# Performance work log

Measured on AMD Instinct MI355X. Metric: run time of the kernel, lower is better.

Reference implementation:

```python
import jax, jax.numpy as jnp
import numpy as np

K = 2
ALPHA = 800.0
TAU = 0.001
MAX_ITER = 50
EPS = 1e-7


def setup_inputs() -> dict:
    key = jax.random.key(0)
    x = jax.random.normal(key, (32, 512, 128), dtype=jnp.float32)
    return {"x": x}


def _vmd(x):
    B, L, D = x.shape
    # fftshift'd frequency grid, broadcast over batch/features: [1, L, 1]
    f_shift = jnp.fft.fftshift(jnp.fft.fftfreq(L).astype(x.dtype))[None, :, None]
    pos_mask = f_shift >= 0
    f_pos = jnp.where(pos_mask, f_shift, 0.0)
    x_hat = jnp.fft.fftshift(jnp.fft.fft(x, axis=1), axes=1)  # [B, L, D] complex

    def body(carry, _):
        u, omega, lam = carry  # u:[B,K,L,D], omega:[B,K,D], lam:[B,L,D]
        # --- mode updates (Wiener filtering in frequency domain) ---
        for k_idx in range(K):
            sum_other = jnp.sum(u, axis=1) - u[:, k_idx]  # sum over modes != k_idx
            sum_other_hat = jnp.fft.fftshift(jnp.fft.fft(sum_other, axis=1), axes=1)
            numerator = x_hat - sum_other_hat + lam / 2
            omega_k = omega[:, k_idx][:, None, :]  # [B,1,D]
            denominator = 1.0 + 2.0 * ALPHA * (f_shift - omega_k) ** 2
            u_hat_k = numerator / denominator
            u_k = jnp.real(jnp.fft.ifft(jnp.fft.ifftshift(u_hat_k, axes=1), axis=1))
            u = u.at[:, k_idx].set(u_k)
        # --- center frequency updates ---
        for k_idx in range(K):
            u_k_hat = jnp.fft.fftshift(jnp.fft.fft(u[:, k_idx], axis=1), axes=1)
            power = jnp.where(pos_mask, jnp.abs(u_k_hat) ** 2, 0.0)  # [B,L,D]
            num_o = jnp.sum(f_pos * power, axis=1)      # [B,D]
            den_o = jnp.sum(power, axis=1) + EPS        # [B,D]
            omega = omega.at[:, k_idx].set(num_o / den_o)
        # --- dual ascent ---
        lam = lam + TAU * (x - jnp.sum(u, axis=1))
        return (u, omega, lam), None

    init = (
        jnp.zeros((B, K, L, D), x.dtype),
        jnp.zeros((B, K, D), x.dtype),
        jnp.zeros((B, L, D), x.dtype),
    )
    (u, omega, _), _ = jax.lax.scan(jax.checkpoint(body), init, None, length=MAX_ITER)

    # sort modes by mean center frequency (ascending) per batch element
    omega_mean = omega.mean(axis=2)                    # [B,K]
    order = jnp.argsort(omega_mean, axis=1)            # [B,K]
    u_sorted = jnp.take_along_axis(u, order[:, :, None, None], axis=1)

    x_trend = jnp.zeros_like(u_sorted[:, 0])
    x_period = u_sorted[:, 0]
    x_res = u_sorted[:, 1]
    return x_trend, x_period, x_res


def reference(x):
    return _vmd(x)
```

## Files before the change

kernel.cpp:

```cpp
#include <hip/hip_runtime.h>
#include <math.h>

#define FIELD 2097152
#define NSEQ  4096

typedef float f2 __attribute__((ext_vector_type(2)));

__device__ __forceinline__ f2 swp(f2 a) { return __builtin_shufflevector(a, a, 1, 0); }
__device__ __forceinline__ f2 conjf2(f2 a) { return (f2){a.x, -a.y}; }
__device__ __forceinline__ f2 cmulp(f2 a, float c, f2 ns)  { return c * a + ns * swp(a); }
__device__ __forceinline__ f2 cmulpc(f2 a, float c, f2 ns) { return c * a - ns * swp(a); }
__device__ __forceinline__ f2 addi(f2 a, f2 b) { return a + (f2){-1.0f, 1.0f} * swp(b); }
__device__ __forceinline__ f2 subi(f2 a, f2 b) { return a + (f2){1.0f, -1.0f} * swp(b); }

template<int CTRL>
__device__ __forceinline__ float dpp_f(float v) {
  return __int_as_float(__builtin_amdgcn_update_dpp(
      __float_as_int(v), __float_as_int(v), CTRL, 0xF, 0xF, true));
}
template<int CTRL>
__device__ __forceinline__ float dpp0_f(float v) {
  return __int_as_float(__builtin_amdgcn_update_dpp(
      0, __float_as_int(v), CTRL, 0xF, 0xF, true));
}
template<int H>
__device__ __forceinline__ float xlane(float v) {
  if constexpr (H == 1)      return dpp_f<0xB1>(v);
  else if constexpr (H == 2) return dpp_f<0x4E>(v);
  else if constexpr (H == 4) return dpp_f<0x141>(dpp_f<0x1B>(v));
  else if constexpr (H == 8) return dpp_f<0x128>(v);
  else return __shfl_xor(v, H, 64);
}
template<int H>
__device__ __forceinline__ f2 xlane2(f2 v) {
  return (f2){xlane<H>(v.x), xlane<H>(v.y)};
}
__device__ __forceinline__ f2 shfl2(f2 v, int l) {
  return (f2){__shfl(v.x, l, 64), __shfl(v.y, l, 64)};
}
__device__ __forceinline__ float bcast0(float v) {
  return __int_as_float(__builtin_amdgcn_readfirstlane(__float_as_int(v)));
}
__device__ __forceinline__ float wave_sum(float v) {
  v += dpp0_f<0x111>(v);
  v += dpp0_f<0x112>(v);
  v += dpp0_f<0x114>(v);
  v += dpp0_f<0x118>(v);
  v += dpp0_f<0x142>(v);
  v += dpp0_f<0x143>(v);
  return __int_as_float(__builtin_amdgcn_readlane(__float_as_int(v), 63));
}

__device__ __forceinline__ void fft4_fwd(f2* v) {
  f2 t0 = v[0] + v[2], t1 = v[0] - v[2];
  f2 t2 = v[1] + v[3], t3 = v[1] - v[3];
  v[0] = t0 + t2; v[2] = t0 - t2;
  v[1] = subi(t1, t3);
  v[3] = addi(t1, t3);
}
__device__ __forceinline__ void fft4_inv(f2* v) {
  f2 t0 = v[0] + v[2], t1 = v[0] - v[2];
  f2 t2 = v[1] + v[3], t3 = v[1] - v[3];
  v[0] = t0 + t2; v[2] = t0 - t2;
  v[1] = addi(t1, t3);
  v[3] = subi(t1, t3);
}

template<int H>
__device__ __forceinline__ void fwd_stage(f2* v, float wr, f2 wn, float sg) {
#pragma unroll
  for (int b = 0; b < 4; ++b) {
    f2 p = xlane2<H>(v[b]);
    f2 t = sg * v[b] + p;
    v[b] = cmulp(t, wr, wn);
  }
}
template<int H>
__device__ __forceinline__ void inv_stage(f2* v, float wr, f2 wn, float sg) {
#pragma unroll
  for (int b = 0; b < 4; ++b) {
    f2 u = cmulpc(v[b], wr, wn);
    f2 p = xlane2<H>(u);
    v[b] = sg * u + p;
  }
}

__device__ __forceinline__ void fft256_fwd(f2* v,
                                           const float* twFc, const f2* twFn,
                                           const float* wrS, const f2* wnS,
                                           const float* sgS) {
  fft4_fwd(v);
#pragma unroll
  for (int b = 1; b < 4; ++b) v[b] = cmulp(v[b], twFc[b-1], twFn[b-1]);
  fwd_stage<32>(v, wrS[0], wnS[0], sgS[0]);
  fwd_stage<16>(v, wrS[1], wnS[1], sgS[1]);
  fwd_stage<8> (v, wrS[2], wnS[2], sgS[2]);
  fwd_stage<4> (v, wrS[3], wnS[3], sgS[3]);
  fwd_stage<2> (v, wrS[4], wnS[4], sgS[4]);
  fwd_stage<1> (v, wrS[5], wnS[5], sgS[5]);
}

__device__ __forceinline__ void ifft256(f2* v,
                                        const float* twFc, const f2* twFn,
                                        const float* wrS, const f2* wnS,
                                        const float* sgS) {
  inv_stage<1> (v, wrS[5], wnS[5], sgS[5]);
  inv_stage<2> (v, wrS[4], wnS[4], sgS[4]);
  inv_stage<4> (v, wrS[3], wnS[3], sgS[3]);
  inv_stage<8> (v, wrS[2], wnS[2], sgS[2]);
  inv_stage<16>(v, wrS[1], wnS[1], sgS[1]);
  inv_stage<32>(v, wrS[0], wnS[0], sgS[0]);
#pragma unroll
  for (int b = 1; b < 4; ++b) v[b] = cmulpc(v[b], twFc[b-1], twFn[b-1]);
  fft4_inv(v);
}

__device__ __forceinline__ void half_to_z(f2* S, float S256,
                                          const float* twHc, const f2* twHn,
                                          int lane, int pl0, int plx) {
  f2 P[4];
  P[0] = shfl2(S[0], pl0);
#pragma unroll
  for (int b = 1; b < 4; ++b) P[b] = shfl2(S[4 - b], plx);
  P[0] = (lane == 0) ? (f2){S256, 0.0f} : P[0];
#pragma unroll
  for (int b = 0; b < 4; ++b) {
    f2 cP = conjf2(P[b]);
    f2 A = 0.5f * (S[b] + cP);
    f2 B = 0.5f * (S[b] - cP);
    f2 Bt = cmulp(B, twHc[b], twHn[b]);
    S[b] = addi(A, Bt);
  }
}

__device__ __forceinline__ void mode_update4(const f2* X, const f2* V, f2* U,
                                             const float* lam1, const float* lam2,
                                             float om, float f0) {
#pragma unroll
  for (int b = 0; b < 4; ++b) {
    float f = f0 + (float)b * (1.0f / 512.0f);
    float dfp = f - om;
    float dfm = f + om;
    float gp = __builtin_amdgcn_rcpf(fmaf(1600.0f * dfp, dfp, 1.0f));
    float gm = __builtin_amdgcn_rcpf(fmaf(1600.0f * dfm, dfm, 1.0f));
    float gs = 0.5f * (gp + gm);
    f2 D = X[b] - V[b];
    float lt = 0.25f * fmaf(lam1[b], gp, lam2[b] * gm);
    U[b] = gs * D + (f2){lt, 0.0f};
  }
}

__global__ __attribute__((amdgpu_flat_work_group_size(256, 256),
                          amdgpu_waves_per_eu(4, 4),
                          amdgpu_num_vgpr(96)))
void vmd_kernel(const float* __restrict__ x, float* __restrict__ out,
                float* __restrict__ ws) {
  __shared__ float stage[4 * 512];
  __shared__ float ldsLam[4 * 512];

  const int tid = threadIdx.x;
  const int wv = tid >> 6;
  const int lane = tid & 63;
  const int w = (blockIdx.x >> 3) + ((blockIdx.x & 7) << 7);
  const int g = 4 * w + wv;
  const int bb = w >> 5;
  const int d0 = (4 * w) & 127;
  const int base4 = bb * 16384 + (d0 >> 2);
  float* lamLds = ldsLam + wv * 512;
  f2* stg2 = (f2*)stage + wv * 256;

  const int rev = (int)(__brev((unsigned)lane) >> 26);
  const float f0 = (float)rev * (1.0f / 128.0f);
  const int plx = lane ^ 63;
  const int pl0 = (int)(__brev((unsigned)((64 - rev) & 63)) >> 26);

  float wrS[6], sgS[6]; f2 wnS[6];
#pragma unroll
  for (int s = 0; s < 6; ++s) {
    const int h = 32 >> s;
    const bool hi = (lane & h) != 0;
    float th = (float)(lane & (h - 1)) * (3.14159265358979323846f / (float)h);
    float sn, cs; sincosf(th, &sn, &cs);
    wrS[s] = hi ? cs : 1.0f;
    wnS[s] = hi ? (f2){sn, -sn} : (f2){0.0f, 0.0f};
    sgS[s] = hi ? -1.0f : 1.0f;
  }
  float twFc[3]; f2 twFn[3];
#pragma unroll
  for (int b = 1; b < 4; ++b) {
    float th = (float)(lane * b) * 0.02454369260617026f;
    float sn, cs; sincosf(th, &sn, &cs);
    twFc[b-1] = cs; twFn[b-1] = (f2){sn, -sn};
  }
  float twHc[4]; f2 twHn[4];
#pragma unroll
  for (int b = 0; b < 4; ++b) {
    float th = (float)(4 * rev + b) * 0.01227184630308513f;
    float sn, cs; sincosf(th, &sn, &cs);
    twHc[b] = cs; twHn[b] = (f2){-sn, sn};
  }

  {
    const float4* x4 = (const float4*)x;
    float4 va = x4[base4 + tid * 32];
    float4 vb = x4[base4 + (tid + 256) * 32];
    stage[tid]        = va.x; stage[512 + tid]        = va.y;
    stage[1024 + tid] = va.z; stage[1536 + tid]       = va.w;
    stage[tid + 256]        = vb.x; stage[512 + tid + 256]  = vb.y;
    stage[1024 + tid + 256] = vb.z; stage[1536 + tid + 256] = vb.w;
#pragma unroll
    for (int j = 0; j < 8; ++j) ldsLam[tid * 8 + j] = 0.0f;
  }
  __syncthreads();

  f2 z[4];
#pragma unroll
  for (int a = 0; a < 4; ++a) z[a] = stg2[64 * a + lane];
  fft256_fwd(z, twFc, twFn, wrS, wnS, sgS);
  f2 X[4];
  float X256;
  {
    f2 P[4];
    P[0] = shfl2(z[0], pl0);
#pragma unroll
    for (int b = 1; b < 4; ++b) P[b] = shfl2(z[4 - b], plx);
    X256 = bcast0(z[0].x - z[0].y);
#pragma unroll
    for (int b = 0; b < 4; ++b) {
      f2 cP = conjf2(P[b]);
      f2 E = 0.5f * (z[b] + cP);
      f2 O = 0.5f * (f2){1.0f, -1.0f} * swp(z[b] - cP);
      X[b] = E + cmulpc(O, twHc[b], twHn[b]);
    }
  }

  f2 U0[4], U1[4], lam[4];
#pragma unroll
  for (int b = 0; b < 4; ++b) {
    U0[b] = (f2){0.0f, 0.0f}; U1[b] = (f2){0.0f, 0.0f};
    lam[b] = (f2){0.0f, 0.0f};
  }
  float U0_256 = 0.0f, U1_256 = 0.0f;
  float om0 = 0.0f, om1 = 0.0f;

  const int psiE = 256 * (lane & 1) + (lane >> 1);

#pragma unroll 1
  for (int it = 0; it < 50; ++it) {
    float lam1[4], lam2[4];
#pragma unroll
    for (int b = 0; b < 4; ++b) lam1[b] = lamLds[128 * b + 64 + rev];
    lam2[0] = lamLds[64 - rev];
#pragma unroll
    for (int b = 1; b < 4; ++b) lam2[b] = lamLds[128 * (4 - b) + 63 - rev];
    float lam0 = lamLds[0];

    mode_update4(X, U1, U0, lam1, lam2, om0, f0);
    {
      float dm = 0.5f + om0;
      float gg = __builtin_amdgcn_rcpf(fmaf(1600.0f * dm, dm, 1.0f));
      U0_256 = (X256 - U1_256 + 0.5f * lam0) * gg;
    }
    mode_update4(X, U0, U1, lam1, lam2, om1, f0);
    {
      float dm = 0.5f + om1;
      float gg = __builtin_amdgcn_rcpf(fmaf(1600.0f * dm, dm, 1.0f));
      U1_256 = (X256 - U0_256 + 0.5f * lam0) * gg;
    }

    f2 s0 = (f2){0.0f, 0.0f}, s1 = (f2){0.0f, 0.0f};
#pragma unroll
    for (int b = 0; b < 4; ++b) {
      float f = f0 + (float)b * (1.0f / 512.0f);
      float p0 = fmaf(U0[b].x, U0[b].x, U0[b].y * U0[b].y);
      float p1 = fmaf(U1[b].x, U1[b].x, U1[b].y * U1[b].y);
      s0 = s0 + (f2){f * p0, p0};
      s1 = s1 + (f2){f * p1, p1};
    }
    float n0 = wave_sum(s0.x), d0s = wave_sum(s0.y);
    float n1 = wave_sum(s1.x), d1s = wave_sum(s1.y);
    om0 = n0 * __builtin_amdgcn_rcpf(d0s + 1e-7f);
    om1 = n1 * __builtin_amdgcn_rcpf(d1s + 1e-7f);

    if (it < 49) {
#pragma unroll
      for (int b = 0; b < 4; ++b) z[b] = U0[b] + U1[b];
      float S256 = U0_256 + U1_256;
      half_to_z(z, S256, twHc, twHn, lane, pl0, plx);
      ifft256(z, twFc, twFn, wrS, wnS, sgS);
#pragma unroll
      for (int a = 0; a < 4; ++a) {
        f2 xa = stg2[64 * a + lane];
        lam[a] = lam[a] + 0.001f * (xa - z[a] * (1.0f / 256.0f));
        lamLds[psiE + 32 * a]       = lam[a].x;
        lamLds[psiE + 32 * a + 128] = lam[a].y;
      }
      asm volatile("s_waitcnt lgkmcnt(0)" ::: "memory");
    }
  }

  float4* o4 = (float4*)out;
#pragma unroll
  for (int b = 0; b < 4; ++b) z[b] = U0[b];
  half_to_z(z, U0_256, twHc, twHn, lane, pl0, plx);
  ifft256(z, twFc, twFn, wrS, wnS, sgS);
  __syncthreads();
#pragma unroll
  for (int a = 0; a < 4; ++a) stg2[64 * a + lane] = z[a] * (1.0f / 256.0f);
  __syncthreads();
#pragma unroll
  for (int r = 0; r < 2; ++r) {
    const int n = tid + r * 256;
    float4 v;
    v.x = stage[n]; v.y = stage[512 + n]; v.z = stage[1024 + n]; v.w = stage[1536 + n];
    o4[FIELD / 4 + base4 + n * 32] = v;
  }
  __syncthreads();
#pragma unroll
  for (int b = 0; b < 4; ++b) z[b] = U1[b];
  half_to_z(z, U1_256, twHc, twHn, lane, pl0, plx);
  ifft256(z, twFc, twFn, wrS, wnS, sgS);
#pragma unroll
  for (int a = 0; a < 4; ++a) stg2[64 * a + lane] = z[a] * (1.0f / 256.0f);
  __syncthreads();
#pragma unroll
  for (int r = 0; r < 2; ++r) {
    const int n = tid + r * 256;
    float4 v;
    v.x = stage[n]; v.y = stage[512 + n]; v.z = stage[1024 + n]; v.w = stage[1536 + n];
    o4[2 * FIELD / 4 + base4 + n * 32] = v;
  }

  if (lane == 0) {
    ws[g] = om0;
    ws[NSEQ + g] = om1;
  }
}

__global__ __launch_bounds__(256) void epi_kernel(float* __restrict__ out,
                                                  const float* __restrict__ ws) {
  const int tid = threadIdx.x;
  const int blk = blockIdx.x;
  const int bb = blk >> 6;
  __shared__ float flagS;
  if (tid < 64) {
    float o0 = ws[bb * 128 + tid] + ws[bb * 128 + 64 + tid];
    float o1 = ws[NSEQ + bb * 128 + tid] + ws[NSEQ + bb * 128 + 64 + tid];
#pragma unroll
    for (int off = 32; off >= 1; off >>= 1) {
      o0 += __shfl_xor(o0, off, 64);
      o1 += __shfl_xor(o1, off, 64);
    }
    if (tid == 0) flagS = (o0 > o1) ? 1.0f : 0.0f;
  }
  __syncthreads();
  const bool sw = flagS > 0.5f;
  float4* o4 = (float4*)out;
  const int i = blk * 256 + tid;
  o4[i] = (float4){0.0f, 0.0f, 0.0f, 0.0f};
  if (sw) {
    float4 p = o4[FIELD / 4 + i];
    float4 r = o4[2 * FIELD / 4 + i];
    o4[FIELD / 4 + i] = r;
    o4[2 * FIELD / 4 + i] = p;
  }
}

extern "C" void kernel_launch(void* const* d_in, const int* in_sizes, int n_in,
                              void* d_out, int out_size, void* d_ws, size_t ws_size,
                              hipStream_t stream) {
  (void)in_sizes; (void)n_in; (void)ws_size; (void)out_size;
  const float* x = (const float*)d_in[0];
  float* out = (float*)d_out;
  float* ws = (float*)d_ws;
  vmd_kernel<<<NSEQ / 4, 256, 0, stream>>>(x, out, ws);
  epi_kernel<<<FIELD / 1024, 256, 0, stream>>>(out, ws);
}
```

Before: 230.0 us.

## Use permlane swaps for wide butterflies, share reciprocal, cache input in registers

Butterfly stages across 32 and 16 lanes now use permlane32/16 swap builtins instead of ds_bpermute-based shuffles. The mode update computes the two Wiener gains from a single reciprocal of the product of the two denominators. The time-domain input is kept in registers so the dual-ascent step no longer re-reads it from LDS, and one barrier before the output staging write is removed. The extra registers held under a 96-VGPR cap could cause spills, and removing the barrier relies on the staging buffer not being read by other waves at that point.

```diff
diff --git a/kernel.cpp b/kernel.cpp
--- a/kernel.cpp
+++ b/kernel.cpp
@@ -34,6 +34,43 @@
 template<int H>
 __device__ __forceinline__ f2 xlane2(f2 v) {
   return (f2){xlane<H>(v.x), xlane<H>(v.y)};
+}
+__device__ __forceinline__ void xsw32(float v, float& a, float& b) {
+#if __has_builtin(__builtin_amdgcn_permlane32_swap)
+  auto r = __builtin_amdgcn_permlane32_swap(__float_as_uint(v), __float_as_uint(v),
+                                            false, false);
+  a = __uint_as_float(r[0]); b = __uint_as_float(r[1]);
+#else
+  float p = __shfl_xor(v, 32, 64);
+  bool hi = (threadIdx.x & 32) != 0;
+  a = hi ? p : v; b = hi ? v : p;
+#endif
+}
+__device__ __forceinline__ void xsw16(float v, float& a, float& b) {
+#if __has_builtin(__builtin_amdgcn_permlane16_swap)
+  auto r = __builtin_amdgcn_permlane16_swap(__float_as_uint(v), __float_as_uint(v),
+                                            false, false);
+  a = __uint_as_float(r[0]); b = __uint_as_float(r[1]);
+#else
+  float p = __shfl_xor(v, 16, 64);
+  bool hi = (threadIdx.x & 16) != 0;
+  a = hi ? p : v; b = hi ? v : p;
+#endif
+}
+template<int H>
+__device__ __forceinline__ f2 bfly2(f2 v, float sg) {
+  if constexpr (H == 32) {
+    float ax, bx, ay, by;
+    xsw32(v.x, ax, bx); xsw32(v.y, ay, by);
+    return (f2){ax, ay} + sg * (f2){bx, by};
+  } else if constexpr (H == 16) {
+    float ax, bx, ay, by;
+    xsw16(v.x, ax, bx); xsw16(v.y, ay, by);
+    return (f2){ax, ay} + sg * (f2){bx, by};
+  } else {
+    f2 p = xlane2<H>(v);
+    return sg * v + p;
+  }
 }
 __device__ __forceinline__ f2 shfl2(f2 v, int l) {
   return (f2){__shfl(v.x, l, 64), __shfl(v.y, l, 64)};
@@ -69,19 +106,15 @@
 template<int H>
 __device__ __forceinline__ void fwd_stage(f2* v, float wr, f2 wn, float sg) {
 #pragma unroll
-  for (int b = 0; b < 4; ++b) {
-    f2 p = xlane2<H>(v[b]);
-    f2 t = sg * v[b] + p;
-    v[b] = cmulp(t, wr, wn);
-  }
+  for (int b = 0; b < 4; ++b)
+    v[b] = cmulp(bfly2<H>(v[b], sg), wr, wn);
 }
 template<int H>
 __device__ __forceinline__ void inv_stage(f2* v, float wr, f2 wn, float sg) {
 #pragma unroll
   for (int b = 0; b < 4; ++b) {
     f2 u = cmulpc(v[b], wr, wn);
-    f2 p = xlane2<H>(u);
-    v[b] = sg * u + p;
+    v[b] = bfly2<H>(u, sg);
   }
 }
 
@@ -141,8 +174,11 @@
     float f = f0 + (float)b * (1.0f / 512.0f);
     float dfp = f - om;
     float dfm = f + om;
-    float gp = __builtin_amdgcn_rcpf(fmaf(1600.0f * dfp, dfp, 1.0f));
-    float gm = __builtin_amdgcn_rcpf(fmaf(1600.0f * dfm, dfm, 1.0f));
+    float Pd = fmaf(1600.0f * dfp, dfp, 1.0f);
+    float Md = fmaf(1600.0f * dfm, dfm, 1.0f);
+    float rr = __builtin_amdgcn_rcpf(Pd * Md);
+    float gp = rr * Md;
+    float gm = rr * Pd;
     float gs = 0.5f * (gp + gm);
     f2 D = X[b] - V[b];
     float lt = 0.25f * fmaf(lam1[b], gp, lam2[b] * gm);
@@ -213,9 +249,9 @@
   }
   __syncthreads();
 
-  f2 z[4];
-#pragma unroll
-  for (int a = 0; a < 4; ++a) z[a] = stg2[64 * a + lane];
+  f2 z[4], xa4[4];
+#pragma unroll
+  for (int a = 0; a < 4; ++a) { z[a] = stg2[64 * a + lane]; xa4[a] = z[a]; }
   fft256_fwd(z, twFc, twFn, wrS, wnS, sgS);
   f2 X[4];
   float X256;
@@ -290,8 +326,7 @@
       ifft256(z, twFc, twFn, wrS, wnS, sgS);
 #pragma unroll
       for (int a = 0; a < 4; ++a) {
-        f2 xa = stg2[64 * a + lane];
-        lam[a] = lam[a] + 0.001f * (xa - z[a] * (1.0f / 256.0f));
+        lam[a] = lam[a] + 0.001f * (xa4[a] - z[a] * (1.0f / 256.0f));
         lamLds[psiE + 32 * a]       = lam[a].x;
         lamLds[psiE + 32 * a + 128] = lam[a].y;
       }
@@ -304,7 +339,6 @@
   for (int b = 0; b < 4; ++b) z[b] = U0[b];
   half_to_z(z, U0_256, twHc, twHn, lane, pl0, plx);
   ifft256(z, twFc, twFn, wrS, wnS, sgS);
-  __syncthreads();
 #pragma unroll
   for (int a = 0; a < 4; ++a) stg2[64 * a + lane] = z[a] * (1.0f / 256.0f);
   __syncthreads();
```

Result: slower. 246.4 us (+7.1%).
